# Kernel tuning notes

Hardware: AMD Instinct MI355X
Metric: run time of the kernel (lower is better)

The kernel has to match this reference:

```python
import jax, jax.numpy as jnp
import numpy as np

B, S, H, NH = 4, 2048, 1024, 16
HD = H // NH
EPS = 1e-12

def setup_inputs() -> dict:
    key = jax.random.key(0)
    ks = jax.random.split(key, 8)
    sc = 1.0 / np.sqrt(H)
    return {
        "input_tensor": jax.random.normal(ks[0], (B, S, H), jnp.float32),
        "attention_mask": jnp.zeros((B, 1, 1, S), jnp.float32),
        "Wq": jax.random.normal(ks[1], (H, H), jnp.float32) * sc,
        "bq": jnp.zeros((H,), jnp.float32),
        "Wk": jax.random.normal(ks[2], (H, H), jnp.float32) * sc,
        "bk": jnp.zeros((H,), jnp.float32),
        "Wv": jax.random.normal(ks[3], (H, H), jnp.float32) * sc,
        "bv": jnp.zeros((H,), jnp.float32),
        "Wo": jax.random.normal(ks[4], (H, H), jnp.float32) * sc,
        "bo": jnp.zeros((H,), jnp.float32),
        "ln_w": jnp.ones((H,), jnp.float32),
        "ln_b": jnpp_zeros if False else jnp.zeros((H,), jnp.float32),
    }

def reference(input_tensor, attention_mask, Wq, bq, Wk, bk, Wv, bv, Wo, bo, ln_w, ln_b):
    x = input_tensor  # [B,S,H]
    # QKV projections (torch Linear: x @ W.T + b), split heads -> [B,S,NH,HD]
    q = (x @ Wq.T + bq).reshape(B, S, NH, HD)
    k = (x @ Wk.T + bk).reshape(B, S, NH, HD)
    v = (x @ Wv.T + bv).reshape(B, S, NH, HD)
    # scores [B,NH,S,S]
    scores = jnp.einsum('bqhd,bkhd->bhqk', q, k) / jnp.sqrt(jnp.float32(HD))
    scores = scores + attention_mask  # broadcast [B,1,1,S]
    probs = jax.nn.softmax(scores, axis=-1)  # dropout is identity in eval
    ctx = jnp.einsum('bhqk,bkhd->bqhd', probs, v).reshape(B, S, H)
    # output dense + residual + LayerNorm (TF-style eps inside sqrt)
    h = ctx @ Wo.T + bo + x
    u = h.mean(-1, keepdims=True)
    s = jnp.mean((h - u) ** 2, axis=-1, keepdims=True)
    return ln_w * (h - u) / jnp.sqrt(s + EPS) + ln_b
```

## Files before the change

### kernel.cpp

```cpp
#include <hip/hip_runtime.h>

typedef __bf16 bf16;
typedef __bf16 bf16x8 __attribute__((ext_vector_type(8)));
typedef __bf16 bf16x4 __attribute__((ext_vector_type(4)));
typedef float floatx4 __attribute__((ext_vector_type(4)));
typedef int   intx4  __attribute__((ext_vector_type(4)));
typedef int   intx2  __attribute__((ext_vector_type(2)));

#define MFMA16(a,b,c) __builtin_amdgcn_mfma_f32_16x16x32_bf16((a),(b),(c),0,0,0)

constexpr int Bc  = 4;
constexpr int Sc  = 2048;
constexpr int Hc  = 1024;
constexpr int NHc = 16;
constexpr int HDc = 64;
constexpr int Mc  = Bc * Sc;
constexpr int KIT = Hc / 32;
constexpr float L2E = 1.44269504088896f;

union U64  { bf16x4 h; intx2 i; };

__device__ __forceinline__ void ld16(const bf16* g, bf16* l) {
    __builtin_amdgcn_global_load_lds(
        (const __attribute__((address_space(1))) void*)g,
        (__attribute__((address_space(3))) void*)l, 16, 0, 0);
}

__global__ void detect_k(const unsigned short* __restrict__ x, int* __restrict__ flag)
{
    if (threadIdx.x == 0 && blockIdx.x == 0) {
        float mx = 0.f;
        for (int i = 0; i < 256; ++i) {
            unsigned int bits = ((unsigned int)x[i]) << 16;
            float v = __uint_as_float(bits);
            if (!isfinite(v)) { mx = 1e30f; break; }
            mx = fmaxf(mx, fabsf(v));
        }
        *flag = (mx > 1e6f) ? 1 : 0;
    }
}

__global__ __launch_bounds__(256)
void conv_all_k(const void* __restrict__ x,
                const void* __restrict__ Wq, const void* __restrict__ Wk,
                const void* __restrict__ Wv, const void* __restrict__ Wo,
                const void* __restrict__ mask,
                const void* __restrict__ bq, const void* __restrict__ bk,
                const void* __restrict__ bv, const void* __restrict__ bo,
                const void* __restrict__ lnw, const void* __restrict__ lnb,
                bf16* __restrict__ xb, bf16* __restrict__ wdst,
                float* maskf, float* bqf, float* bkf, float* bvf,
                float* bof, float* lnwf, float* lnbf,
                const int* __restrict__ flag)
{
    const int g = blockIdx.x * 256 + threadIdx.x;
    const int fl = *flag;
    if (g < 1048576) {
        if (fl) {
            const float* s = (const float*)x + (size_t)g * 8;
            union { intx4 v; bf16 e[8]; } o;
#pragma unroll
            for (int j = 0; j < 8; ++j) o.e[j] = (bf16)s[j];
            *(intx4*)(xb + (size_t)g * 8) = o.v;
        } else {
            *(intx4*)(xb + (size_t)g * 8) = *((const intx4*)x + g);
        }
    } else if (g < 1048576 + 524288) {
        const int gw = g - 1048576;
        const int wsel = gw >> 17, go = gw & 131071;
        const void* s = (wsel == 0) ? Wq : (wsel == 1) ? Wk : (wsel == 2) ? Wv : Wo;
        if (fl) {
            const float* sp = (const float*)s + (size_t)go * 8;
            union { intx4 v; bf16 e[8]; } o;
#pragma unroll
            for (int j = 0; j < 8; ++j) o.e[j] = (bf16)sp[j];
            *(intx4*)(wdst + (size_t)gw * 8) = o.v;
        } else {
            *(intx4*)(wdst + (size_t)gw * 8) = *((const intx4*)s + go);
        }
    } else {
        const int gs = g - 1048576 - 524288;
        if (gs >= 1792) return;
        const void* src; float* dst; int off; float scl = 1.0f;
        if (gs < 1024) { src = mask; dst = maskf; off = gs * 8; scl = L2E; }
        else {
            const int a = (gs - 1024) >> 7;
            off = ((gs - 1024) & 127) * 8;
            switch (a) {
                case 0: src = bq;  dst = bqf;  break;
                case 1: src = bk;  dst = bkf;  break;
                case 2: src = bv;  dst = bvf;  break;
                case 3: src = bo;  dst = bof;  break;
                case 4: src = lnw; dst = lnwf; break;
                default: src = lnb; dst = lnbf; break;
            }
        }
        if (fl) {
            const float* s = (const float*)src + off;
#pragma unroll
            for (int j = 0; j < 8; ++j) dst[off + j] = s[j] * scl;
        } else {
            union { intx4 v; bf16 e[8]; } u;
            u.v = *(const intx4*)((const bf16*)src + off);
#pragma unroll
            for (int j = 0; j < 8; ++j) dst[off + j] = (float)u.e[j] * scl;
        }
    }
}

template<int SWAP>
__device__ __forceinline__
void gemm_core(const bf16* __restrict__ A, const bf16* __restrict__ W,
               int m0, int n0, int t, bf16* As, bf16* Bs, floatx4 (&acc)[4][4])
{
    const int l  = t & 63, w = t >> 6;
    const int wr = w >> 1, wc = w & 1;
    const int lq = l >> 4, ln = l & 15;
    const int srow = t >> 2;
    const int scol = (t & 3) * 8;

    const bf16* a0 = A + (size_t)(m0 + srow) * Hc + scol;
    const bf16* b0 = W + (size_t)(n0 + srow) * Hc + scol;
    const int dst = srow * 32 + scol;

    auto stage = [&](int buf, int kb) {
        const int off = kb * 32;
        bf16* dA = As + buf * 4096;
        bf16* dB = Bs + buf * 4096;
        ld16(a0 + off,           dA + dst);
        ld16(a0 + 64 * Hc + off, dA + 64 * 32 + dst);
        ld16(b0 + off,           dB + dst);
        ld16(b0 + 64 * Hc + off, dB + 64 * 32 + dst);
    };

    stage(0, 0);
    int cur = 0;
    for (int kb = 0; kb < KIT; ++kb) {
        __syncthreads();
        if (kb + 1 < KIT) stage(cur ^ 1, kb + 1);

        const bf16* Ab = As + cur * 4096;
        const bf16* Bb = Bs + cur * 4096;
        bf16x8 af[4], bw[4];
#pragma unroll
        for (int i = 0; i < 4; ++i)
            af[i] = *(const bf16x8*)&Ab[(wr * 64 + i * 16 + ln) * 32 + lq * 8];
#pragma unroll
        for (int j = 0; j < 4; ++j)
            bw[j] = *(const bf16x8*)&Bb[(wc * 64 + j * 16 + ln) * 32 + lq * 8];

        __builtin_amdgcn_s_setprio(1);
#pragma unroll
        for (int i = 0; i < 4; ++i)
#pragma unroll
            for (int j = 0; j < 4; ++j)
                acc[i][j] = SWAP ? MFMA16(bw[j], af[i], acc[i][j])
                                 : MFMA16(af[i], bw[j], acc[i][j]);
        __builtin_amdgcn_s_setprio(0);
        cur ^= 1;
    }
}

__device__ __forceinline__ void xcd_remap(int bx, int by, int& m0, int& n0)
{
    const int flat = by * 8 + bx;
    const int sw   = (flat & 7) * 64 + (flat >> 3);
    m0 = (sw >> 3) * 128;
    n0 = (sw & 7) * 128;
}

__global__ __launch_bounds__(256)
void qkv_gemm(const bf16* __restrict__ x,
              const bf16* __restrict__ Wq, const float* __restrict__ bq,
              const bf16* __restrict__ Wk, const float* __restrict__ bk,
              const bf16* __restrict__ Wv, const float* __restrict__ bv,
              bf16* __restrict__ qo, bf16* __restrict__ ko, bf16* __restrict__ vto)
{
    __shared__ __align__(16) bf16 smem[16384];
    const int z = blockIdx.z;
    const bf16*  W    = (z == 0) ? Wq : (z == 1) ? Wk : Wv;
    const float* bias = (z == 0) ? bq : (z == 1) ? bk : bv;

    int m0, n0;
    xcd_remap(blockIdx.x, blockIdx.y, m0, n0);
    const int t  = threadIdx.x;
    const int l  = t & 63, w = t >> 6;
    const int wr = w >> 1, wc = w & 1;
    const int lq = l >> 4, ln = l & 15;

    if (z < 2) {
        floatx4 acc[4][4] = {};
        gemm_core<1>(x, W, m0, n0, t, smem, smem + 8192, acc);
        bf16* out = (z == 0) ? qo : ko;
        const float sc = (z == 0) ? 0.125f * L2E : 1.0f;
#pragma unroll
        for (int j = 0; j < 4; ++j) {
            const int feat = n0 + wc * 64 + j * 16 + lq * 4;
            const floatx4 bb = *(const floatx4*)&bias[feat];
            const int hh = feat >> 6, dd = feat & 63;
#pragma unroll
            for (int i = 0; i < 4; ++i) {
                const int xrow = m0 + wr * 64 + i * 16 + ln;
                const int bi = xrow >> 11, si = xrow & (Sc - 1);
                U64 pk;
#pragma unroll
                for (int r = 0; r < 4; ++r) pk.h[r] = (bf16)((acc[i][j][r] + bb[r]) * sc);
                *(intx2*)&out[(((size_t)bi * NHc + hh) * Sc + si) * HDc + dd] = pk.i;
            }
        }
    } else {
        floatx4 acc[4][4] = {};
        gemm_core<0>(x, W, m0, n0, t, smem, smem + 8192, acc);
        bf16* Ct = smem;
        const int bi = m0 >> 11, s0 = m0 & (Sc - 1);
        for (int h2 = 0; h2 < 2; ++h2) {
            __syncthreads();
            if (wc == h2) {
#pragma unroll
                for (int j = 0; j < 4; ++j) {
                    const int c = j * 16 + ln;
                    const float bb = bias[n0 + h2 * 64 + c];
#pragma unroll
                    for (int i = 0; i < 4; ++i) {
                        U64 pk;
#pragma unroll
                        for (int r = 0; r < 4; ++r) pk.h[r] = (bf16)(acc[i][j][r] + bb);
                        *(intx2*)&Ct[c * 136 + wr * 64 + i * 16 + lq * 4] = pk.i;
                    }
                }
            }
            __syncthreads();
#pragma unroll
            for (int u = 0; u < 4; ++u) {
                const int id = t + 256 * u;
                const int c = id >> 4, rg = id & 15;
                const int hh = (n0 >> 6) + h2;
                intx4 val = *(const intx4*)&Ct[c * 136 + rg * 8];
                *(intx4*)&vto[(((size_t)bi * NHc + hh) * HDc + c) * Sc + s0 + rg * 8] = val;
            }
        }
    }
}

__global__ __launch_bounds__(256)
void oproj_gemm(const bf16* __restrict__ ctx, const bf16* __restrict__ Wo,
                const float* __restrict__ bo, const bf16* __restrict__ xb,
                bf16* __restrict__ hout)
{
    __shared__ __align__(16) bf16 smem[16384];
    int m0, n0;
    xcd_remap(blockIdx.x, blockIdx.y, m0, n0);
    const int t  = threadIdx.x;
    floatx4 acc[4][4] = {};
    gemm_core<1>(ctx, Wo, m0, n0, t, smem, smem + 8192, acc);

    const int l  = t & 63, w = t >> 6;
    const int wr = w >> 1, wc = w & 1;
    const int lq = l >> 4, ln = l & 15;
#pragma unroll
    for (int j = 0; j < 4; ++j) {
        const int col = n0 + wc * 64 + j * 16 + lq * 4;
        const floatx4 bb = *(const floatx4*)&bo[col];
#pragma unroll
        for (int i = 0; i < 4; ++i) {
            const int row = m0 + wr * 64 + i * 16 + ln;
            U64 rx;
            rx.i = *(const intx2*)&xb[(size_t)row * Hc + col];
            U64 pk;
#pragma unroll
            for (int r = 0; r < 4; ++r)
                pk.h[r] = (bf16)(acc[i][j][r] + bb[r] + (float)rx.h[r]);
            *(intx2*)&hout[(size_t)row * Hc + col] = pk.i;
        }
    }
}

__global__ __launch_bounds__(256, 2)
void attention(const bf16* __restrict__ q, const bf16* __restrict__ k,
               const bf16* __restrict__ vt, const float* __restrict__ maskf,
               bf16* __restrict__ ctx)
{
    __shared__ __align__(16) bf16 Ks[2][64][64];
    __shared__ __align__(16) bf16 Pt[256][72];

    const int raw = blockIdx.x;
    const int xcd = raw & 7, jj = raw >> 3;
    const int bh  = xcd * 8 + (jj >> 3);
    const int qt  = jj & 7;
    const int b = bh >> 4, h = bh & 15;
    const int t = threadIdx.x, w = t >> 6, l = t & 63;
    const int lq = l >> 4, ln = l & 15;
    const int q0 = qt * 256 + w * 64;

    const bf16* kg = k  + (size_t)bh * Sc * HDc;
    const bf16* vg = vt + (size_t)bh * HDc * Sc;
    const float* mbase = maskf + b * Sc;

    const int rr  = l >> 3;
    const int gsw = ((l & 7) ^ rr) << 3;
    const int r0  = w * 16 + rr, r1 = r0 + 8;
    const int dco = (l & 7) << 3;
    const int sw  = ln & 7;

    bf16x8 qf[4][2];
#pragma unroll
    for (int qb = 0; qb < 4; ++qb)
#pragma unroll
        for (int kh = 0; kh < 2; ++kh)
            qf[qb][kh] = *(const bf16x8*)(q + ((size_t)bh * Sc + q0 + qb * 16 + ln) * HDc
                                            + kh * 32 + lq * 8);

    floatx4 o[4][4] = {};
    float dacc[4] = {0.f, 0.f, 0.f, 0.f};
    floatx4 s[4][4];
    bf16x8 vf[4][2];

    auto stageK = [&](int buf, int kt) {
        bf16* Kd = &Ks[buf][0][0];
        ld16(kg + (size_t)(kt * 64 + r0) * HDc + gsw, Kd + r0 * 64 + dco);
        ld16(kg + (size_t)(kt * 64 + r1) * HDc + gsw, Kd + r1 * 64 + dco);
    };
    auto loadV = [&](int kt) {
#pragma unroll
        for (int db = 0; db < 4; ++db)
#pragma unroll
            for (int kh = 0; kh < 2; ++kh)
                vf[db][kh] = *(const bf16x8*)(vg + (size_t)(db * 16 + ln) * Sc
                                                + kt * 64 + kh * 32 + lq * 8);
    };
    auto doQKT = [&](int kt, int cur) {
        floatx4 mvl[4];
#pragma unroll
        for (int cb = 0; cb < 4; ++cb)
            mvl[cb] = *(const floatx4*)(mbase + kt * 64 + cb * 16 + lq * 4);
        bf16x8 kf[4][2];
#pragma unroll
        for (int cb = 0; cb < 4; ++cb)
#pragma unroll
            for (int kh = 0; kh < 2; ++kh)
                kf[cb][kh] = *(const bf16x8*)&Ks[cur][cb * 16 + ln]
                                               [((kh * 4 + lq) ^ sw) << 3];
#pragma unroll
        for (int qb = 0; qb < 4; ++qb)
#pragma unroll
            for (int cb = 0; cb < 4; ++cb)
                s[qb][cb] = mvl[cb];
        __builtin_amdgcn_s_setprio(1);
#pragma unroll
        for (int kh = 0; kh < 2; ++kh)
#pragma unroll
            for (int qb = 0; qb < 4; ++qb)
#pragma unroll
                for (int cb = 0; cb < 4; ++cb)
                    s[qb][cb] = MFMA16(kf[cb][kh], qf[qb][kh], s[qb][cb]);
        __builtin_amdgcn_s_setprio(0);
    };
    auto doPV = [&]() {
        __builtin_amdgcn_s_setprio(1);
#pragma unroll
        for (int qb = 0; qb < 4; ++qb) {
            const bf16x8 pf0 = *(const bf16x8*)&Pt[w * 64 + qb * 16 + ln][lq * 8];
            const bf16x8 pf1 = *(const bf16x8*)&Pt[w * 64 + qb * 16 + ln][32 + lq * 8];
#pragma unroll
            for (int db = 0; db < 4; ++db) {
                o[qb][db] = MFMA16(vf[db][0], pf0, o[qb][db]);
                o[qb][db] = MFMA16(vf[db][1], pf1, o[qb][db]);
            }
        }
        __builtin_amdgcn_s_setprio(0);
    };
    auto doSoftmax = [&]() {
#pragma unroll
        for (int qb = 0; qb < 4; ++qb) {
            float ds = 0.f;
#pragma unroll
            for (int cb = 0; cb < 4; ++cb) {
                U64 pk;
#pragma unroll
                for (int r = 0; r < 4; ++r) {
                    const float e = __builtin_amdgcn_exp2f(s[qb][cb][r]);
                    ds += e;
                    pk.h[r] = (bf16)e;
                }
                *(intx2*)&Pt[w * 64 + qb * 16 + ln][cb * 16 + lq * 4] = pk.i;
            }
            dacc[qb] += ds;
        }
    };

    stageK(0, 0);
    loadV(0);
    int cur = 0;

    __syncthreads();
    stageK(1, 1);
    doQKT(0, 0);
    doSoftmax();
    cur = 1;

    for (int kt = 1; kt < Sc / 64; ++kt) {
        __syncthreads();
        if (kt + 1 < Sc / 64) stageK(cur ^ 1, kt + 1);
        doQKT(kt, cur);
        doPV();
        loadV(kt);
        doSoftmax();
        cur ^= 1;
    }
    doPV();

#pragma unroll
    for (int qb = 0; qb < 4; ++qb) {
        float dsum = dacc[qb];
        dsum += __shfl_xor(dsum, 16, 64);
        dsum += __shfl_xor(dsum, 32, 64);
        const float li = 1.f / dsum;
        const int qg = q0 + qb * 16 + ln;
#pragma unroll
        for (int db = 0; db < 4; ++db) {
            U64 pk;
#pragma unroll
            for (int r = 0; r < 4; ++r) pk.h[r] = (bf16)(o[qb][db][r] * li);
            *(intx2*)&ctx[((size_t)b * Sc + qg) * Hc + h * HDc + db * 16 + lq * 4] = pk.i;
        }
    }
}

__global__ __launch_bounds__(256)
void layernorm_k(const bf16* __restrict__ hbuf, const float* __restrict__ lw,
                 const float* __restrict__ lb, void* __restrict__ outp,
                 const int* __restrict__ flag)
{
    const int row = blockIdx.x;
    const int t = threadIdx.x;
    const bf16* hp = hbuf + (size_t)row * Hc;

    union { intx2 i2; bf16 e[4]; } pk;
    pk.i2 = *(const intx2*)(hp + t * 4);
    float v[4], sum = 0.f, sq = 0.f;
#pragma unroll
    for (int i = 0; i < 4; ++i) {
        v[i] = (float)pk.e[i];
        sum += v[i];
        sq  += v[i] * v[i];
    }
#pragma unroll
    for (int off = 1; off < 64; off <<= 1) {
        sum += __shfl_xor(sum, off, 64);
        sq  += __shfl_xor(sq,  off, 64);
    }
    __shared__ float ssum[4], ssq[4];
    const int w = t >> 6;
    if ((t & 63) == 0) { ssum[w] = sum; ssq[w] = sq; }
    __syncthreads();
    sum = ssum[0] + ssum[1] + ssum[2] + ssum[3];
    sq  = ssq[0]  + ssq[1]  + ssq[2]  + ssq[3];

    const float mean = sum * (1.f / (float)Hc);
    const float var  = sq * (1.f / (float)Hc) - mean * mean;
    const float rstd = rsqrtf(var + 1e-12f);

    float ov[4];
#pragma unroll
    for (int i = 0; i < 4; ++i) {
        const int c = t * 4 + i;
        ov[i] = lw[c] * (v[i] - mean) * rstd + lb[c];
    }
    if (*flag) {
        float* of = (float*)outp + (size_t)row * Hc + t * 4;
#pragma unroll
        for (int i = 0; i < 4; ++i) of[i] = ov[i];
    } else {
        union { intx2 i2; bf16 e[4]; } po;
#pragma unroll
        for (int i = 0; i < 4; ++i) po.e[i] = (bf16)ov[i];
        *(intx2*)((bf16*)outp + (size_t)row * Hc + t * 4) = po.i2;
    }
}

extern "C" void kernel_launch(void* const* d_in, const int* in_sizes, int n_in,
                              void* d_out, int out_size, void* d_ws, size_t ws_size,
                              hipStream_t stream)
{
    const void* x    = d_in[0];
    const void* mask = d_in[1];
    const void* Wq   = d_in[2];
    const void* bq   = d_in[3];
    const void* Wk   = d_in[4];
    const void* bk   = d_in[5];
    const void* Wv   = d_in[6];
    const void* bv   = d_in[7];
    const void* Wo   = d_in[8];
    const void* bo   = d_in[9];
    const void* lnw  = d_in[10];
    const void* lnb  = d_in[11];

    char* ws = (char*)d_ws;
    const size_t MB = 1024 * 1024;
    int*   flag  = (int*)ws;
    float* maskf = (float*)(ws + 4096);
    float* bqf   = (float*)(ws + 64 * 1024);
    float* bkf   = bqf + Hc;
    float* bvf   = bkf + Hc;
    float* bof   = bvf + Hc;
    float* lnwf  = bof + Hc;
    float* lnbf  = lnwf + Hc;
    bf16* xb  = (bf16*)(ws + 1 * MB);
    bf16* wqb = (bf16*)(ws + 17 * MB);
    bf16* wkb = (bf16*)(ws + 19 * MB);
    bf16* wvb = (bf16*)(ws + 21 * MB);
    bf16* wob = (bf16*)(ws + 23 * MB);
    bf16* qb  = (bf16*)(ws + 25 * MB);
    bf16* kb  = (bf16*)(ws + 41 * MB);
    bf16* vtb = (bf16*)(ws + 57 * MB);
    bf16* cb  = (bf16*)(ws + 73 * MB);
    bf16* hb  = qb;

    detect_k<<<1, 64, 0, stream>>>((const unsigned short*)x, flag);

    conv_all_k<<<6153, 256, 0, stream>>>(x, Wq, Wk, Wv, Wo, mask,
                                         bq, bk, bv, bo, lnw, lnb,
                                         xb, wqb, maskf, bqf, bkf, bvf,
                                         bof, lnwf, lnbf, flag);

    dim3 gqkv(Hc / 128, Mc / 128, 3);
    qkv_gemm<<<gqkv, 256, 0, stream>>>(xb, wqb, bqf, wkb, bkf, wvb, bvf, qb, kb, vtb);
    attention<<<dim3(Bc * NHc * (Sc / 256)), 256, 0, stream>>>(qb, kb, vtb, maskf, cb);
    oproj_gemm<<<dim3(Hc / 128, Mc / 128), 256, 0, stream>>>(cb, wob, bof, xb, hb);
    layernorm_k<<<dim3(Mc), 256, 0, stream>>>(hb, lnwf, lnbf, d_out, flag);
}
```

Measured before the change: 340.9 us.

## Stage V tiles through LDS and restructure attention loop per query block

V tiles are now double-buffered into shared memory with async global-to-LDS loads alongside K, instead of being read from global memory straight into registers. The software pipeline that overlapped P·V of the previous tile with QK^T of the current one is replaced by a simpler per-iteration QK^T, softmax, P·V sequence, with the score accumulators scoped per query block to cut register pressure. The P buffer becomes per-wave 64x64 with an XOR swizzle in place of padding. This trades the cross-tile overlap for lower VGPR use and LDS-sourced V, and uses more LDS, which may limit occupancy.

```diff
diff --git a/kernel.cpp b/kernel.cpp
--- a/kernel.cpp
+++ b/kernel.cpp
@@ -281,7 +281,8 @@
                bf16* __restrict__ ctx)
 {
     __shared__ __align__(16) bf16 Ks[2][64][64];
-    __shared__ __align__(16) bf16 Pt[256][72];
+    __shared__ __align__(16) bf16 Vs[2][64][64];
+    __shared__ __align__(16) bf16 Pt[4][64][64];
 
     const int raw = blockIdx.x;
     const int xcd = raw & 7, jj = raw >> 3;
@@ -301,6 +302,7 @@
     const int r0  = w * 16 + rr, r1 = r0 + 8;
     const int dco = (l & 7) << 3;
     const int sw  = ln & 7;
+    const int pkey = sw << 1;
 
     bf16x8 qf[4][2];
 #pragma unroll
@@ -312,27 +314,29 @@
 
     floatx4 o[4][4] = {};
     float dacc[4] = {0.f, 0.f, 0.f, 0.f};
-    floatx4 s[4][4];
-    bf16x8 vf[4][2];
-
-    auto stageK = [&](int buf, int kt) {
+
+    auto stage = [&](int buf, int kt) {
         bf16* Kd = &Ks[buf][0][0];
+        bf16* Vd = &Vs[buf][0][0];
         ld16(kg + (size_t)(kt * 64 + r0) * HDc + gsw, Kd + r0 * 64 + dco);
         ld16(kg + (size_t)(kt * 64 + r1) * HDc + gsw, Kd + r1 * 64 + dco);
+        ld16(vg + (size_t)r0 * Sc + kt * 64 + gsw,    Vd + r0 * 64 + dco);
+        ld16(vg + (size_t)r1 * Sc + kt * 64 + gsw,    Vd + r1 * 64 + dco);
     };
-    auto loadV = [&](int kt) {
-#pragma unroll
-        for (int db = 0; db < 4; ++db)
-#pragma unroll
-            for (int kh = 0; kh < 2; ++kh)
-                vf[db][kh] = *(const bf16x8*)(vg + (size_t)(db * 16 + ln) * Sc
-                                                + kt * 64 + kh * 32 + lq * 8);
-    };
-    auto doQKT = [&](int kt, int cur) {
+
+    stage(0, 0);
+    int cur = 0;
+    bf16* PtW = &Pt[w][0][0];
+
+    for (int kt = 0; kt < Sc / 64; ++kt) {
+        __syncthreads();
+        if (kt + 1 < Sc / 64) stage(cur ^ 1, kt + 1);
+
         floatx4 mvl[4];
 #pragma unroll
         for (int cb = 0; cb < 4; ++cb)
             mvl[cb] = *(const floatx4*)(mbase + kt * 64 + cb * 16 + lq * 4);
+
         bf16x8 kf[4][2];
 #pragma unroll
         for (int cb = 0; cb < 4; ++cb)
@@ -340,74 +344,59 @@
             for (int kh = 0; kh < 2; ++kh)
                 kf[cb][kh] = *(const bf16x8*)&Ks[cur][cb * 16 + ln]
                                                [((kh * 4 + lq) ^ sw) << 3];
-#pragma unroll
-        for (int qb = 0; qb < 4; ++qb)
-#pragma unroll
-            for (int cb = 0; cb < 4; ++cb)
-                s[qb][cb] = mvl[cb];
-        __builtin_amdgcn_s_setprio(1);
-#pragma unroll
-        for (int kh = 0; kh < 2; ++kh)
-#pragma unroll
-            for (int qb = 0; qb < 4; ++qb)
+
+#pragma unroll
+        for (int qb = 0; qb < 4; ++qb) {
+            floatx4 s[4];
+#pragma unroll
+            for (int cb = 0; cb < 4; ++cb) s[cb] = mvl[cb];
+            __builtin_amdgcn_s_setprio(1);
+#pragma unroll
+            for (int kh = 0; kh < 2; ++kh)
 #pragma unroll
                 for (int cb = 0; cb < 4; ++cb)
-                    s[qb][cb] = MFMA16(kf[cb][kh], qf[qb][kh], s[qb][cb]);
-        __builtin_amdgcn_s_setprio(0);
-    };
-    auto doPV = [&]() {
-        __builtin_amdgcn_s_setprio(1);
+                    s[cb] = MFMA16(kf[cb][kh], qf[qb][kh], s[cb]);
+            __builtin_amdgcn_s_setprio(0);
+            float ds = 0.f;
+#pragma unroll
+            for (int cb = 0; cb < 4; ++cb) {
+                U64 pk;
+#pragma unroll
+                for (int r = 0; r < 4; ++r) {
+                    const float e = __builtin_amdgcn_exp2f(s[cb][r]);
+                    ds += e;
+                    pk.h[r] = (bf16)e;
+                }
+                *(intx2*)(PtW + (qb * 16 + ln) * 64
+                              + (((cb * 4 + lq) ^ pkey) << 2)) = pk.i;
+            }
+            dacc[qb] += ds;
+        }
+
+        bf16x8 vf[4][2];
+#pragma unroll
+        for (int db = 0; db < 4; ++db)
+#pragma unroll
+            for (int kh = 0; kh < 2; ++kh)
+                vf[db][kh] = *(const bf16x8*)&Vs[cur][db * 16 + ln]
+                                               [((kh * 4 + lq) ^ sw) << 3];
+
 #pragma unroll
         for (int qb = 0; qb < 4; ++qb) {
-            const bf16x8 pf0 = *(const bf16x8*)&Pt[w * 64 + qb * 16 + ln][lq * 8];
-            const bf16x8 pf1 = *(const bf16x8*)&Pt[w * 64 + qb * 16 + ln][32 + lq * 8];
+            const bf16x8 pf0 = *(const bf16x8*)(PtW + (qb * 16 + ln) * 64
+                                                    + (((2 * lq) ^ pkey) << 2));
+            const bf16x8 pf1 = *(const bf16x8*)(PtW + (qb * 16 + ln) * 64
+                                                    + (((8 + 2 * lq) ^ pkey) << 2));
+            __builtin_amdgcn_s_setprio(1);
 #pragma unroll
             for (int db = 0; db < 4; ++db) {
                 o[qb][db] = MFMA16(vf[db][0], pf0, o[qb][db]);
                 o[qb][db] = MFMA16(vf[db][1], pf1, o[qb][db]);
             }
-        }
-        __builtin_amdgcn_s_setprio(0);
-    };
-    auto doSoftmax = [&]() {
-#pragma unroll
-        for (int qb = 0; qb < 4; ++qb) {
-            float ds = 0.f;
-#pragma unroll
-            for (int cb = 0; cb < 4; ++cb) {
-                U64 pk;
-#pragma unroll
-                for (int r = 0; r < 4; ++r) {
-                    const float e = __builtin_amdgcn_exp2f(s[qb][cb][r]);
-                    ds += e;
-                    pk.h[r] = (bf16)e;
-                }
-                *(intx2*)&Pt[w * 64 + qb * 16 + ln][cb * 16 + lq * 4] = pk.i;
-            }
-            dacc[qb] += ds;
-        }
-    };
-
-    stageK(0, 0);
-    loadV(0);
-    int cur = 0;
-
-    __syncthreads();
-    stageK(1, 1);
-    doQKT(0, 0);
-    doSoftmax();
-    cur = 1;
-
-    for (int kt = 1; kt < Sc / 64; ++kt) {
-        __syncthreads();
-        if (kt + 1 < Sc / 64) stageK(cur ^ 1, kt + 1);
-        doQKT(kt, cur);
-        doPV();
-        loadV(kt);
-        doSoftmax();
+            __builtin_amdgcn_s_setprio(0);
+        }
         cur ^= 1;
     }
-    doPV();
 
 #pragma unroll
     for (int qb = 0; qb < 4; ++qb) {
```

Result: no change. 338.8 us (-0.6%).
